# Optimization experiments

Hardware: AMD Instinct MI355X
Metric: run time of the kernel (lower is better)

## Reference

```python
import jax, jax.numpy as jnp
import numpy as np

D = 1024   # feature_dim
K = 10     # num_anchors
B = 16384  # batch
H = 8      # num_heads


def setup_inputs() -> dict:
    key = jax.random.key(0)
    ks = jax.random.split(key, 12)
    f32 = jnp.float32

    def w(k, shape, scale=0.02):
        return (jax.random.normal(k, shape, f32) * scale)

    return {
        "features": jax.random.normal(ks[0], (B, D), f32),
        "anchors": w(ks[1], (K, D), 0.1),
        # anchor_refiner: Linear(D, D//2) -> ReLU -> Linear(D//2, D) -> Tanh
        "ar_w1": w(ks[2], (D, D // 2)), "ar_b1": jnp.zeros((D // 2,), f32),
        "ar_w2": w(ks[3], (D // 2, D)), "ar_b2": jnp.zeros((D,), f32),
        # attention projections
        "q_w": w(ks[4], (D, D)), "q_b": jnp.zeros((D,), f32),
        "k_w": w(ks[5], (D, D)), "k_b": jnp.zeros((D,), f32),
        "v_w": w(ks[6], (D, D)), "v_b": jnp.zeros((D,), f32),
        "o_w": w(ks[7], (D, D)), "o_b": jnp.zeros((D,), f32),
        # feature_enhancer: LayerNorm -> Linear(D,2D) -> GELU -> Linear(2D,D)
        "ln_g": jnp.ones((D,), f32), "ln_b": jnp.zeros((D,), f32),
        "ff_w1": w(ks[8], (D, 2 * D)), "ff_b1": jnp.zeros((2 * D,), f32),
        "ff_w2": w(ks[9], (2 * D, D)), "ff_b2": jnp.zeros((D,), f32),
        "div_w": jnp.asarray(0.001, f32),
        "cen_w": jnp.asarray(0.001, f32),
    }


def _l2norm(x, eps=1e-8):
    n = jnp.linalg.norm(x, axis=-1, keepdims=True)
    return x / jnp.maximum(n, eps)


def _layernorm(x, g, b, eps=1e-5):
    mu = jnp.mean(x, axis=-1, keepdims=True)
    var = jnp.mean(jnp.square(x - mu), axis=-1, keepdims=True)
    return (x - mu) * jax.lax.rsqrt(var + eps) * g + b


def reference(features, anchors, ar_w1, ar_b1, ar_w2, ar_b2,
              q_w, q_b, k_w, k_b, v_w, v_b, o_w, o_b,
              ln_g, ln_b, ff_w1, ff_b1, ff_w2, ff_b2, div_w, cen_w):
    b = features.shape[0]
    hd = D // H
    fn = _l2norm(features)                                 # [B, D]

    # anchor refinement
    refin = jnp.tanh(jax.nn.relu(anchors @ ar_w1 + ar_b1) @ ar_w2 + ar_b2)
    an = _l2norm(anchors + 0.1 * refin)                    # [K, D]

    # multi-head cross-attention to anchors
    q = (fn @ q_w + q_b).reshape(b, H, hd)                 # [B, H, hd]
    k = (an @ k_w + k_b).reshape(K, H, hd)                 # [K, H, hd]
    v = (an @ v_w + v_b).reshape(K, H, hd)
    scores = jnp.einsum('bhd,khd->bhk', q, k) / jnp.sqrt(jnp.asarray(hd, fn.dtype))
    aw = jax.nn.softmax(scores, axis=-1)                   # [B, H, K]
    att = jnp.einsum('bhk,khd->bhd', aw, v).reshape(b, D)
    att = att @ o_w + o_b

    # feature enhancer (dropout inactive: eval mode)
    enh = fn + 0.1 * att
    h = jax.nn.gelu(_layernorm(enh, ln_g, ln_b) @ ff_w1 + ff_b1, approximate=False)
    enh = h @ ff_w2 + ff_b2
    final = fn + 0.2 * enh                                 # [B, D]

    # diversity loss: pdist over K=10 anchors (45 pairs)
    diff = an[:, None, :] - an[None, :, :]                 # [K, K, D]
    dmat = jnp.sqrt(jnp.maximum(jnp.sum(diff * diff, -1), 1e-24))
    iu = np.triu_indices(K, 1)
    div_loss = jnp.exp(-jnp.maximum(dmat[iu].mean(), 1e-6))

    # center loss: attention-weighted feature-anchor distances
    avg_att = aw.mean(axis=1)                              # [B, K]
    sq = (jnp.sum(fn * fn, 1, keepdims=True) + jnp.sum(an * an, 1)
          - 2.0 * fn @ an.T)
    fa_dist = jnp.sqrt(jnp.maximum(sq, 1e-12))             # [B, K]
    center_loss = jnp.sum(avg_att * fa_dist, axis=1).mean()

    geo = jnp.abs(div_w) * div_loss + jnp.abs(cen_w) * center_loss
    geo = jnp.clip(geo, 0.0, 0.01)
    return final, geo
```

## Files before the change

### kernel.cpp

```cpp
#include <hip/hip_runtime.h>
#include <hip/hip_bf16.h>
#include <math.h>

typedef __hip_bfloat16 bf16;

#define D_  1024
#define K_  10
#define B_  16384
#define H_  8
#define HD_ 128

struct alignas(16) BF8 { bf16 v[8]; };
struct alignas(8)  BF4 { bf16 v[4]; };

typedef __bf16 bf8v __attribute__((ext_vector_type(8)));
typedef float  f4v  __attribute__((ext_vector_type(4)));

__device__ __forceinline__ float b2f(bf16 x){ return __bfloat162float(x); }
__device__ __forceinline__ bf16  f2b(float x){ return __float2bfloat16(x); }

#define GL2LDS16(g, l) __builtin_amdgcn_global_load_lds( \
    (__attribute__((address_space(1))) void*)(g), \
    (__attribute__((address_space(3))) void*)(l), 16, 0, 0)

__global__ __launch_bounds__(256) void l2norm_k(const float* __restrict__ x,
                                                bf16* __restrict__ fnb) {
  int b = blockIdx.x, t = threadIdx.x;
  float4 v = ((const float4*)(x + (size_t)b * D_))[t];
  float p = v.x*v.x + v.y*v.y + v.z*v.z + v.w*v.w;
  #pragma unroll
  for (int o = 32; o > 0; o >>= 1) p += __shfl_down(p, o);
  __shared__ float wsum[4];
  if ((t & 63) == 0) wsum[t >> 6] = p;
  __syncthreads();
  __shared__ float inv_s;
  if (t == 0) inv_s = 1.f / fmaxf(sqrtf(wsum[0]+wsum[1]+wsum[2]+wsum[3]), 1e-8f);
  __syncthreads();
  float iv = inv_s;
  BF4 o;
  o.v[0] = f2b(v.x*iv); o.v[1] = f2b(v.y*iv);
  o.v[2] = f2b(v.z*iv); o.v[3] = f2b(v.w*iv);
  ((BF4*)(fnb + (size_t)b * D_))[t] = o;
}

__global__ __launch_bounds__(256) void wt_k(const float* __restrict__ w,
                                            bf16* __restrict__ wt, int R, int C) {
  __shared__ float tle[32][33];
  int c0 = blockIdx.x * 32, r0 = blockIdx.y * 32;
  int tx = threadIdx.x & 31, ty = threadIdx.x >> 5;
  #pragma unroll
  for (int i = 0; i < 32; i += 8)
    tle[ty + i][tx] = w[(size_t)(r0 + ty + i) * C + c0 + tx];
  __syncthreads();
  #pragma unroll
  for (int i = 0; i < 32; i += 8)
    wt[(size_t)(c0 + ty + i) * R + r0 + tx] = f2b(tle[tx][ty + i]);
}

template<int COLS, int KD, int ACT>
__global__ __launch_bounds__(256) void panelmm_k(
    const float* __restrict__ A, const float* __restrict__ W,
    const float* __restrict__ bias, const float* __restrict__ aux,
    float* __restrict__ out,
    const float* __restrict__ W2, const float* __restrict__ bias2,
    float* __restrict__ out2, int N, int npanel) {
  constexpr int GROUPS = 256 / COLS;
  constexpr int DCH = KD / GROUPS;
  __shared__ float A_s[K_][KD];
  __shared__ float part[K_][COLS][GROUPS];
  const int t = threadIdx.x;
  int blk = blockIdx.x;
  const float* Wm = W; const float* bm = bias; float* om = out;
  if (blk >= npanel) { blk -= npanel; Wm = W2; bm = bias2; om = out2; }
  const int panel = blk;
  for (int i = t; i < K_*KD; i += 256) A_s[0][i] = A[i];
  __syncthreads();
  const int cg = t % COLS, g = t / COLS;
  const int col = panel*COLS + cg;
  float s[K_];
  #pragma unroll
  for (int r = 0; r < K_; ++r) s[r] = 0.f;
  const float* wp = Wm + (size_t)(g*DCH)*N + col;
  for (int d = g*DCH; d < (g+1)*DCH; ++d) {
    float wv = *wp; wp += N;
    #pragma unroll
    for (int r = 0; r < K_; ++r) s[r] = fmaf(A_s[r][d], wv, s[r]);
  }
  #pragma unroll
  for (int r = 0; r < K_; ++r) part[r][cg][g] = s[r];
  __syncthreads();
  for (int o = t; o < K_*COLS; o += 256) {
    int r = o / COLS, c = o % COLS;
    float v = 0.f;
    #pragma unroll
    for (int gg = 0; gg < GROUPS; ++gg) v += part[r][c][gg];
    v += bm[panel*COLS + c];
    if constexpr (ACT == 1) v = fmaxf(v, 0.f);
    if constexpr (ACT == 2) v = aux[(size_t)r*N + panel*COLS + c] + 0.1f*tanhf(v);
    om[(size_t)r*N + panel*COLS + c] = v;
  }
}

template<int TRANSOUT, typename TW>
__global__ __launch_bounds__(256) void smallmm_k(
    const float* __restrict__ A, const TW* __restrict__ W,
    bf16* __restrict__ outb, float scale) {
  constexpr int COLS = 64, GROUPS = 4, DCH = 32, NW = 1024;
  __shared__ float A_s[K_][128];
  __shared__ float part[K_][COLS][GROUPS];
  const int t = threadIdx.x;
  const int h = blockIdx.x & 7, panel = blockIdx.x >> 3;
  for (int i = t; i < K_*128; i += 256) {
    int r = i >> 7, j = i & 127;
    A_s[r][j] = A[r*1024 + h*128 + j];
  }
  __syncthreads();
  const int cg = t % COLS, g = t / COLS;
  const int col = panel*COLS + cg;
  float s[K_];
  #pragma unroll
  for (int r = 0; r < K_; ++r) s[r] = 0.f;
  const TW* wp = W + (size_t)(h*128 + g*DCH)*NW + col;
  for (int d = g*DCH; d < g*DCH + DCH; ++d) {
    float wv;
    if constexpr (sizeof(TW) == 2) wv = b2f(*wp); else wv = *wp;
    wp += NW;
    #pragma unroll
    for (int r = 0; r < K_; ++r) s[r] = fmaf(A_s[r][d], wv, s[r]);
  }
  #pragma unroll
  for (int r = 0; r < K_; ++r) part[r][cg][g] = s[r];
  __syncthreads();
  for (int o = t; o < 16*COLS; o += 256) {
    int r = o / COLS, c = o % COLS;
    float v = 0.f;
    if (r < K_) {
      #pragma unroll
      for (int gg = 0; gg < GROUPS; ++gg) v += part[r][c][gg];
      v *= scale;
    }
    if constexpr (TRANSOUT) outb[(size_t)(panel*COLS + c)*128 + h*16 + r] = f2b(v);
    else                    outb[(size_t)(h*16 + r)*NW + panel*COLS + c] = f2b(v);
  }
}

__global__ void sbias_k(const float* __restrict__ qb, const float* __restrict__ Km,
                        const float* __restrict__ na, float* __restrict__ sb) {
  int c = threadIdx.x;
  if (c < 128) {
    int h = c >> 4, k = c & 15;
    float s = 0.f;
    if (k < K_) {
      for (int j = 0; j < HD_; ++j)
        s = fmaf(qb[h*HD_ + j], Km[(size_t)k*D_ + h*HD_ + j], s);
    }
    sb[c] = s * 0.08838834764831845f;
  } else {
    int j = c - 128;
    sb[c] = (j < K_) ? (1.f + na[j]) : 0.f;
  }
}

__global__ __launch_bounds__(256) void anext_k(const float* __restrict__ an,
                                               bf16* __restrict__ wt) {
  int k = blockIdx.x;
  bf16* dst = wt + (size_t)(128 + k) * 1024;
  int i = threadIdx.x * 4;
  BF4 o;
  if (k < K_) {
    float4 a = *(const float4*)(an + (size_t)k*1024 + i);
    o.v[0] = f2b(-2.f*a.x); o.v[1] = f2b(-2.f*a.y);
    o.v[2] = f2b(-2.f*a.z); o.v[3] = f2b(-2.f*a.w);
  } else {
    o.v[0] = o.v[1] = o.v[2] = o.v[3] = f2b(0.f);
  }
  *(BF4*)(dst + i) = o;
}

__global__ __launch_bounds__(256) void ar3_k(const float* __restrict__ an_un,
    float* __restrict__ an, float* __restrict__ na, float* __restrict__ divloss) {
  __shared__ float a_s[K_][D_];
  __shared__ float nrm[K_];
  __shared__ float dm[45];
  const int t = threadIdx.x;
  for (int i = t; i < K_*D_; i += 256) a_s[0][i] = an_un[i];
  __syncthreads();
  const int wid = t >> 6, lane = t & 63;
  for (int r = wid; r < K_; r += 4) {
    float p = 0.f;
    for (int j = lane; j < D_; j += 64) p += a_s[r][j]*a_s[r][j];
    #pragma unroll
    for (int o = 1; o < 64; o <<= 1) p += __shfl_xor(p, o);
    if (lane == 0) nrm[r] = p;
  }
  __syncthreads();
  for (int i = t; i < K_*D_; i += 256) {
    int r = i >> 10;
    float iv = 1.f / fmaxf(sqrtf(nrm[r]), 1e-8f);
    float v = a_s[0][i] * iv;
    a_s[0][i] = v;
    an[i] = v;
  }
  if (t < K_) {
    float iv = 1.f / fmaxf(sqrtf(nrm[t]), 1e-8f);
    na[t] = nrm[t] * iv * iv;
  }
  __syncthreads();
  const int pr = t >> 2, sub = t & 3;
  if (pr < 45) {
    int i = 0, j = 0, c = pr;
    for (i = 0; i < K_; ++i) { int cnt = K_-1-i; if (c < cnt) { j = i+1+c; break; } c -= cnt; }
    float s = 0.f;
    for (int d = sub*256; d < sub*256 + 256; ++d) {
      float df = a_s[i][d] - a_s[j][d]; s += df*df;
    }
    s += __shfl_xor(s, 1); s += __shfl_xor(s, 2);
    if (sub == 0) dm[pr] = sqrtf(fmaxf(s, 1e-24f));
  }
  __syncthreads();
  if (t == 0) {
    float m = 0.f;
    for (int p = 0; p < 45; ++p) m += dm[p];
    m *= (1.f/45.f);
    *divloss = expf(-fmaxf(m, 1e-6f));
  }
}

template<int EPI, typename TO>
__global__ __launch_bounds__(256) void mgemm_k(
    const bf16* __restrict__ A, const bf16* __restrict__ Bt,
    const float* __restrict__ bias, const bf16* __restrict__ aux,
    TO* __restrict__ out, int M, int N, int Kd, float scale) {
  constexpr int BM = 128, BN = 128, BK = 32;
  __shared__ bf16 As[BM][BK];
  __shared__ bf16 Bs[BN][BK];
  const int tid = threadIdx.x;
  const int nMB = M / BM;
  const int nwg = gridDim.x;
  int wg = blockIdx.x;
  wg = (wg & 7) * (nwg >> 3) + (wg >> 3);
  const int mb = wg % nMB, nb = wg / nMB;
  const int bm = mb * BM, bn = nb * BN;

  const int srow = tid >> 2;
  const int sk   = (tid & 3) * 8;
  const bf16* ga = A  + (size_t)(bm + srow) * Kd + sk;
  const bf16* gb = Bt + (size_t)(bn + srow) * Kd + sk;
  const size_t rstep = (size_t)64 * Kd;
  bf16* la = &As[0][0] + tid * 8;
  bf16* lb = &Bs[0][0] + tid * 8;

  const int w    = tid >> 6;
  const int lane = tid & 63;
  const int wr = (w >> 1) * 64, wc = (w & 1) * 64;
  const int fr = lane & 15, fg = lane >> 4;

  f4v acc[4][4];
  const f4v zz = {0.f, 0.f, 0.f, 0.f};
  #pragma unroll
  for (int m = 0; m < 4; ++m)
    #pragma unroll
    for (int n = 0; n < 4; ++n) acc[m][n] = zz;

  for (int k0 = 0; k0 < Kd; k0 += BK) {
    GL2LDS16(ga,         la);
    GL2LDS16(ga + rstep, la + 2048);
    GL2LDS16(gb,         lb);
    GL2LDS16(gb + rstep, lb + 2048);
    __syncthreads();
    bf8v af[4], bf_[4];
    #pragma unroll
    for (int m = 0; m < 4; ++m)
      af[m] = *(const bf8v*)&As[wr + m*16 + fr][fg*8];
    #pragma unroll
    for (int n = 0; n < 4; ++n)
      bf_[n] = *(const bf8v*)&Bs[wc + n*16 + fr][fg*8];
    #pragma unroll
    for (int m = 0; m < 4; ++m)
      #pragma unroll
      for (int n = 0; n < 4; ++n)
        acc[m][n] = __builtin_amdgcn_mfma_f32_16x16x32_bf16(af[m], bf_[n], acc[m][n], 0, 0, 0);
    __syncthreads();
    ga += BK; gb += BK;
  }

  float bv[4];
  #pragma unroll
  for (int n = 0; n < 4; ++n) bv[n] = bias[bn + wc + n*16 + fr];
  #pragma unroll
  for (int m = 0; m < 4; ++m) {
    #pragma unroll
    for (int r = 0; r < 4; ++r) {
      const int row = bm + wr + m*16 + fg*4 + r;
      #pragma unroll
      for (int n = 0; n < 4; ++n) {
        const int col = bn + wc + n*16 + fr;
        float x = acc[m][n][r] + bv[n];
        if constexpr (EPI == 1) x = b2f(aux[(size_t)row * N + col]) + scale * x;
        if constexpr (EPI == 2) x = 0.5f * x * (1.f + erff(x * 0.70710678118654752f));
        if constexpr (sizeof(TO) == 2) out[(size_t)row * N + col] = f2b(x);
        else                           out[(size_t)row * N + col] = x;
      }
    }
  }
}

template<int EPI, typename TO>
__global__ __launch_bounds__(512) void mgemm256_k(
    const bf16* __restrict__ A, const bf16* __restrict__ Bt,
    const float* __restrict__ bias, const bf16* __restrict__ aux,
    TO* __restrict__ out, int M, int N, int Kd, float scale) {
  constexpr int BM = 256, BN = 256, BK = 64;
  __shared__ bf16 As[2][BM*BK];
  __shared__ bf16 Bs[2][BN*BK];
  const int tid = threadIdx.x;
  const int nMB = M / BM;
  const int nwg = gridDim.x;
  int wg = blockIdx.x;
  wg = (wg & 7) * (nwg >> 3) + (wg >> 3);
  const int bm = (wg % nMB) * BM, bn = (wg / nMB) * BN;

  const int srow = tid >> 3;
  const int scsw = ((tid & 7) ^ (srow & 7)) * 8;
  const bf16* gA = A  + (size_t)(bm + srow) * Kd + scsw;
  const bf16* gB = Bt + (size_t)(bn + srow) * Kd + scsw;
  const size_t lstep = (size_t)64 * Kd;

  const int wid = tid >> 6, lane = tid & 63;
  const int wm = wid >> 2, wn = wid & 3;
  const int fr = lane & 15, fg = lane >> 4;
  const int fsw = fr & 7;

  f4v acc[8][4];
  const f4v zz = {0.f, 0.f, 0.f, 0.f};
  #pragma unroll
  for (int m = 0; m < 8; ++m)
    #pragma unroll
    for (int n = 0; n < 4; ++n) acc[m][n] = zz;

  const int nt = Kd / BK;

  #pragma unroll
  for (int l = 0; l < 4; ++l) {
    GL2LDS16(gA + l*lstep, &As[0][0] + tid*8 + l*4096);
    GL2LDS16(gB + l*lstep, &Bs[0][0] + tid*8 + l*4096);
  }
  __syncthreads();

  int buf = 0;
  for (int t = 0; t < nt; ++t) {
    if (t + 1 < nt) {
      const int ko = (t + 1) * BK;
      #pragma unroll
      for (int l = 0; l < 4; ++l) {
        GL2LDS16(gA + l*lstep + ko, &As[buf^1][0] + tid*8 + l*4096);
        GL2LDS16(gB + l*lstep + ko, &Bs[buf^1][0] + tid*8 + l*4096);
      }
    }
    const bf16* la = &As[buf][0];
    const bf16* lb = &Bs[buf][0];
    bf8v bq[8];
    #pragma unroll
    for (int n = 0; n < 4; ++n) {
      const int rb = wn*64 + n*16 + fr;
      bq[n*2]   = *(const bf8v*)(lb + rb*64 + ((fg     ^ fsw) * 8));
      bq[n*2+1] = *(const bf8v*)(lb + rb*64 + (((4+fg) ^ fsw) * 8));
    }
    __builtin_amdgcn_s_setprio(1);
    #pragma unroll
    for (int m = 0; m < 8; ++m) {
      const int ra = wm*128 + m*16 + fr;
      bf8v a0 = *(const bf8v*)(la + ra*64 + ((fg     ^ fsw) * 8));
      bf8v a1 = *(const bf8v*)(la + ra*64 + (((4+fg) ^ fsw) * 8));
      #pragma unroll
      for (int n = 0; n < 4; ++n) {
        acc[m][n] = __builtin_amdgcn_mfma_f32_16x16x32_bf16(a0, bq[n*2],   acc[m][n], 0, 0, 0);
        acc[m][n] = __builtin_amdgcn_mfma_f32_16x16x32_bf16(a1, bq[n*2+1], acc[m][n], 0, 0, 0);
      }
    }
    __builtin_amdgcn_s_setprio(0);
    __syncthreads();
    buf ^= 1;
  }

  float bv[4];
  #pragma unroll
  for (int n = 0; n < 4; ++n) bv[n] = bias[bn + wn*64 + n*16 + fr];
  #pragma unroll
  for (int m = 0; m < 8; ++m) {
    #pragma unroll
    for (int r = 0; r < 4; ++r) {
      const int row = bm + wm*128 + m*16 + fg*4 + r;
      #pragma unroll
      for (int n = 0; n < 4; ++n) {
        const int col = bn + wn*64 + n*16 + fr;
        float x = acc[m][n][r] + bv[n];
        if constexpr (EPI == 1) x = b2f(aux[(size_t)row * N + col]) + scale * x;
        if constexpr (EPI == 2) x = 0.5f * x * (1.f + erff(x * 0.70710678118654752f));
        if constexpr (sizeof(TO) == 2) out[(size_t)row * N + col] = f2b(x);
        else                           out[(size_t)row * N + col] = x;
      }
    }
  }
}

__global__ __launch_bounds__(256) void attn2_k(
    const float* __restrict__ S, bf16* __restrict__ awp,
    float* __restrict__ cen_acc) {
  __shared__ float cred[4];
  const int t = threadIdx.x;
  const int wid = t >> 6, lane = t & 63;
  const int sub = lane & 7, head = lane >> 3;
  const int k0 = sub*2, k1 = k0 + 1;
  float c_acc = 0.f;
  const int row0 = blockIdx.x * 32 + wid * 8;

  for (int i = 0; i < 8; ++i) {
    const int row = row0 + i;
    const float* Sr = S + (size_t)row * 256;
    float2 sv = *(const float2*)(Sr + head*16 + k0);
    float v0 = (k0 < K_) ? sv.x : -1e30f;
    float v1 = (k1 < K_) ? sv.y : -1e30f;
    float m = fmaxf(v0, v1);
    m = fmaxf(m, __shfl_xor(m,1)); m = fmaxf(m, __shfl_xor(m,2)); m = fmaxf(m, __shfl_xor(m,4));
    float e0 = (k0 < K_) ? __expf(v0 - m) : 0.f;
    float e1 = (k1 < K_) ? __expf(v1 - m) : 0.f;
    float es = e0 + e1;
    es += __shfl_xor(es,1); es += __shfl_xor(es,2); es += __shfl_xor(es,4);
    float inv = 1.f / es;
    float a0 = e0 * inv, a1 = e1 * inv;
    bf16 b0 = f2b(a0), b1 = f2b(a1);
    unsigned int pk = (unsigned int)(*(unsigned short*)&b0)
                    | ((unsigned int)(*(unsigned short*)&b1) << 16);
    *(unsigned int*)(awp + (size_t)row*128 + head*16 + k0) = pk;
    float g0 = a0, g1 = a1;
    g0 += __shfl_xor(g0,8); g0 += __shfl_xor(g0,16); g0 += __shfl_xor(g0,32);
    g1 += __shfl_xor(g1,8); g1 += __shfl_xor(g1,16); g1 += __shfl_xor(g1,32);
    if (sub < 5) {
      float d20 = Sr[128 + k0];
      float d21 = Sr[128 + k1];
      c_acc = fmaf(g0, sqrtf(fmaxf(d20, 1e-12f)), c_acc);
      c_acc = fmaf(g1, sqrtf(fmaxf(d21, 1e-12f)), c_acc);
    }
  }
  #pragma unroll
  for (int o = 1; o < 64; o <<= 1) c_acc += __shfl_xor(c_acc, o);
  if (lane == 0) cred[wid] = c_acc;
  __syncthreads();
  if (t == 0) {
    float s = (cred[0]+cred[1]+cred[2]+cred[3]) * (1.f/64.f/(float)B_);
    atomicAdd(cen_acc, s);
  }
}

__global__ __launch_bounds__(256) void ln_k(const bf16* __restrict__ x,
    const float* __restrict__ g, const float* __restrict__ bta,
    bf16* __restrict__ out) {
  int b = blockIdx.x, t = threadIdx.x;
  BF4 ld = ((const BF4*)(x + (size_t)b * D_))[t];
  float v[4];
  #pragma unroll
  for (int j = 0; j < 4; ++j) v[j] = b2f(ld.v[j]);
  float s = v[0]+v[1]+v[2]+v[3];
  #pragma unroll
  for (int o = 32; o > 0; o >>= 1) s += __shfl_down(s, o);
  __shared__ float w1[4], w2[4];
  if ((t & 63) == 0) w1[t >> 6] = s;
  __syncthreads();
  __shared__ float mu_s, rs_s;
  if (t == 0) mu_s = (w1[0]+w1[1]+w1[2]+w1[3]) * (1.f/D_);
  __syncthreads();
  float mu = mu_s;
  float qv = 0.f;
  #pragma unroll
  for (int j = 0; j < 4; ++j) { float d = v[j]-mu; qv += d*d; }
  #pragma unroll
  for (int o = 32; o > 0; o >>= 1) qv += __shfl_down(qv, o);
  if ((t & 63) == 0) w2[t >> 6] = qv;
  __syncthreads();
  if (t == 0) rs_s = rsqrtf((w2[0]+w2[1]+w2[2]+w2[3]) * (1.f/D_) + 1e-5f);
  __syncthreads();
  float rs = rs_s;
  BF4 o;
  #pragma unroll
  for (int j = 0; j < 4; ++j) {
    int col = t*4 + j;
    o.v[j] = f2b((v[j]-mu)*rs*g[col] + bta[col]);
  }
  ((BF4*)(out + (size_t)b * D_))[t] = o;
}

__global__ void geo_k(const float* __restrict__ divl, const float* __restrict__ cen,
                      const float* __restrict__ div_w, const float* __restrict__ cen_w,
                      float* __restrict__ out) {
  float g = fabsf(*div_w) * (*divl) + fabsf(*cen_w) * (*cen);
  out[0] = fminf(fmaxf(g, 0.f), 0.01f);
}

extern "C" void kernel_launch(void* const* d_in, const int* in_sizes, int n_in,
                              void* d_out, int out_size, void* d_ws, size_t ws_size,
                              hipStream_t stream) {
  const float* features = (const float*)d_in[0];
  const float* anchors  = (const float*)d_in[1];
  const float* ar_w1 = (const float*)d_in[2];
  const float* ar_b1 = (const float*)d_in[3];
  const float* ar_w2 = (const float*)d_in[4];
  const float* ar_b2 = (const float*)d_in[5];
  const float* q_w = (const float*)d_in[6];
  const float* q_b = (const float*)d_in[7];
  const float* k_w = (const float*)d_in[8];
  const float* k_b = (const float*)d_in[9];
  const float* v_w = (const float*)d_in[10];
  const float* v_b = (const float*)d_in[11];
  const float* o_w = (const float*)d_in[12];
  const float* o_b = (const float*)d_in[13];
  const float* ln_g = (const float*)d_in[14];
  const float* ln_b = (const float*)d_in[15];
  const float* ff_w1 = (const float*)d_in[16];
  const float* ff_b1 = (const float*)d_in[17];
  const float* ff_w2 = (const float*)d_in[18];
  const float* ff_b2 = (const float*)d_in[19];
  const float* div_w = (const float*)d_in[20];
  const float* cen_w = (const float*)d_in[21];
  float* out = (float*)d_out;

  char* w = (char*)d_ws;
  bf16* ws_fnb = (bf16*)w;  w += (size_t)B_ * D_ * 2;
  bf16* ws_enh = (bf16*)w;  w += (size_t)B_ * D_ * 2;
  bf16* ws_ln  = (bf16*)w;  w += (size_t)B_ * D_ * 2;
  bf16* ws_h   = (bf16*)w;  w += (size_t)B_ * 2048 * 2;
  float* ws_S  = (float*)w; w += (size_t)B_ * 256 * 4;
  bf16* ws_awp = (bf16*)w;  w += (size_t)B_ * 128 * 2;
  bf16* ws_wq  = (bf16*)w;  w += (size_t)D_ * D_ * 2;
  bf16* ws_w1t = (bf16*)w;  w += (size_t)D_ * 2048 * 2;
  bf16* ws_w2t = (bf16*)w;  w += (size_t)2048 * D_ * 2;
  bf16* ws_wt  = (bf16*)w;  w += (size_t)256 * D_ * 2;
  bf16* ws_vt  = (bf16*)w;  w += (size_t)D_ * 128 * 2;
  float* ws_har = (float*)w;  w += (size_t)K_ * (D_/2) * 4;
  float* ws_anu = (float*)w;  w += (size_t)K_ * D_ * 4;
  float* ws_an  = (float*)w;  w += (size_t)K_ * D_ * 4;
  float* ws_k   = (float*)w;  w += (size_t)K_ * D_ * 4;
  float* ws_v   = (float*)w;  w += (size_t)K_ * D_ * 4;
  float* ws_na  = (float*)w;  w += 256;
  float* ws_div = (float*)w;  w += 256;
  float* ws_cen = (float*)w;  w += 256;
  float* ws_sb  = (float*)w;  w += 512;
  if ((size_t)(w - (char*)d_ws) > ws_size) return;

  hipMemsetAsync(ws_cen, 0, 4, stream);

  wt_k<<<dim3(D_/32,   D_/32),   256, 0, stream>>>(q_w,   ws_wq,  D_,   D_);
  wt_k<<<dim3(2048/32, D_/32),   256, 0, stream>>>(ff_w1, ws_w1t, D_,   2048);
  wt_k<<<dim3(D_/32,   2048/32), 256, 0, stream>>>(ff_w2, ws_w2t, 2048, D_);

  l2norm_k<<<B_, 256, 0, stream>>>(features, ws_fnb);

  panelmm_k<32, 1024, 1><<<16, 256, 0, stream>>>(
      anchors, ar_w1, ar_b1, nullptr, ws_har,
      nullptr, nullptr, nullptr, D_/2, 16);
  panelmm_k<64, 512, 2><<<16, 256, 0, stream>>>(
      ws_har, ar_w2, ar_b2, anchors, ws_anu,
      nullptr, nullptr, nullptr, D_, 16);
  ar3_k<<<1, 256, 0, stream>>>(ws_anu, ws_an, ws_na, ws_div);
  panelmm_k<64, 1024, 0><<<32, 256, 0, stream>>>(
      ws_an, k_w, k_b, nullptr, ws_k,
      v_w, v_b, ws_v, D_, 16);

  smallmm_k<0, bf16><<<128, 256, 0, stream>>>(ws_k, ws_wq, ws_wt, 0.08838834764831845f);
  anext_k<<<128, 256, 0, stream>>>(ws_an, ws_wt);
  sbias_k<<<1, 256, 0, stream>>>(q_b, ws_k, ws_na, ws_sb);
  smallmm_k<1, float><<<128, 256, 0, stream>>>(ws_v, o_w, ws_vt, 1.f);

  mgemm_k<0, float><<<dim3((B_/128)*(256/128)), 256, 0, stream>>>(
      ws_fnb, ws_wt, ws_sb, nullptr, ws_S, B_, 256, D_, 0.f);

  attn2_k<<<B_/32, 256, 0, stream>>>(ws_S, ws_awp, ws_cen);

  mgemm256_k<1, bf16><<<dim3((B_/256)*(D_/256)), 512, 0, stream>>>(
      ws_awp, ws_vt, o_b, ws_fnb, ws_enh, B_, D_, 128, 0.1f);

  ln_k<<<B_, 256, 0, stream>>>(ws_enh, ln_g, ln_b, ws_ln);

  mgemm256_k<2, bf16><<<dim3((B_/256)*(2048/256)), 512, 0, stream>>>(
      ws_ln, ws_w1t, ff_b1, nullptr, ws_h, B_, 2048, D_, 0.f);

  mgemm256_k<1, float><<<dim3((B_/256)*(D_/256)), 512, 0, stream>>>(
      ws_h, ws_w2t, ff_b2, ws_fnb, out, B_, D_, 2048, 0.2f);

  geo_k<<<1, 1, 0, stream>>>(ws_div, ws_cen, div_w, cen_w, out + (size_t)B_ * D_);
}
```

Before: 420.0 us.

## Replace 256x256 GEMM with double-buffered swizzled 128x128 tile kernel

Removes the 256x256x64 MFMA GEMM and rewrites the 128x128x32 kernel with LDS double buffering and an XOR swizzle to reduce bank conflicts. The three large GEMMs (out-proj, FF1, FF2) now launch the smaller-tile kernel with 256 threads. This aims for higher occupancy and more workgroups, at the cost of halving per-tile data reuse and adding more global and LDS traffic per FLOP.

```diff
diff --git a/kernel.cpp b/kernel.cpp
--- a/kernel.cpp
+++ b/kernel.cpp
@@ -232,85 +232,6 @@
     const float* __restrict__ bias, const bf16* __restrict__ aux,
     TO* __restrict__ out, int M, int N, int Kd, float scale) {
   constexpr int BM = 128, BN = 128, BK = 32;
-  __shared__ bf16 As[BM][BK];
-  __shared__ bf16 Bs[BN][BK];
-  const int tid = threadIdx.x;
-  const int nMB = M / BM;
-  const int nwg = gridDim.x;
-  int wg = blockIdx.x;
-  wg = (wg & 7) * (nwg >> 3) + (wg >> 3);
-  const int mb = wg % nMB, nb = wg / nMB;
-  const int bm = mb * BM, bn = nb * BN;
-
-  const int srow = tid >> 2;
-  const int sk   = (tid & 3) * 8;
-  const bf16* ga = A  + (size_t)(bm + srow) * Kd + sk;
-  const bf16* gb = Bt + (size_t)(bn + srow) * Kd + sk;
-  const size_t rstep = (size_t)64 * Kd;
-  bf16* la = &As[0][0] + tid * 8;
-  bf16* lb = &Bs[0][0] + tid * 8;
-
-  const int w    = tid >> 6;
-  const int lane = tid & 63;
-  const int wr = (w >> 1) * 64, wc = (w & 1) * 64;
-  const int fr = lane & 15, fg = lane >> 4;
-
-  f4v acc[4][4];
-  const f4v zz = {0.f, 0.f, 0.f, 0.f};
-  #pragma unroll
-  for (int m = 0; m < 4; ++m)
-    #pragma unroll
-    for (int n = 0; n < 4; ++n) acc[m][n] = zz;
-
-  for (int k0 = 0; k0 < Kd; k0 += BK) {
-    GL2LDS16(ga,         la);
-    GL2LDS16(ga + rstep, la + 2048);
-    GL2LDS16(gb,         lb);
-    GL2LDS16(gb + rstep, lb + 2048);
-    __syncthreads();
-    bf8v af[4], bf_[4];
-    #pragma unroll
-    for (int m = 0; m < 4; ++m)
-      af[m] = *(const bf8v*)&As[wr + m*16 + fr][fg*8];
-    #pragma unroll
-    for (int n = 0; n < 4; ++n)
-      bf_[n] = *(const bf8v*)&Bs[wc + n*16 + fr][fg*8];
-    #pragma unroll
-    for (int m = 0; m < 4; ++m)
-      #pragma unroll
-      for (int n = 0; n < 4; ++n)
-        acc[m][n] = __builtin_amdgcn_mfma_f32_16x16x32_bf16(af[m], bf_[n], acc[m][n], 0, 0, 0);
-    __syncthreads();
-    ga += BK; gb += BK;
-  }
-
-  float bv[4];
-  #pragma unroll
-  for (int n = 0; n < 4; ++n) bv[n] = bias[bn + wc + n*16 + fr];
-  #pragma unroll
-  for (int m = 0; m < 4; ++m) {
-    #pragma unroll
-    for (int r = 0; r < 4; ++r) {
-      const int row = bm + wr + m*16 + fg*4 + r;
-      #pragma unroll
-      for (int n = 0; n < 4; ++n) {
-        const int col = bn + wc + n*16 + fr;
-        float x = acc[m][n][r] + bv[n];
-        if constexpr (EPI == 1) x = b2f(aux[(size_t)row * N + col]) + scale * x;
-        if constexpr (EPI == 2) x = 0.5f * x * (1.f + erff(x * 0.70710678118654752f));
-        if constexpr (sizeof(TO) == 2) out[(size_t)row * N + col] = f2b(x);
-        else                           out[(size_t)row * N + col] = x;
-      }
-    }
-  }
-}
-
-template<int EPI, typename TO>
-__global__ __launch_bounds__(512) void mgemm256_k(
-    const bf16* __restrict__ A, const bf16* __restrict__ Bt,
-    const float* __restrict__ bias, const bf16* __restrict__ aux,
-    TO* __restrict__ out, int M, int N, int Kd, float scale) {
-  constexpr int BM = 256, BN = 256, BK = 64;
   __shared__ bf16 As[2][BM*BK];
   __shared__ bf16 Bs[2][BN*BK];
   const int tid = threadIdx.x;
@@ -320,64 +241,57 @@
   wg = (wg & 7) * (nwg >> 3) + (wg >> 3);
   const int bm = (wg % nMB) * BM, bn = (wg / nMB) * BN;
 
-  const int srow = tid >> 3;
-  const int scsw = ((tid & 7) ^ (srow & 7)) * 8;
-  const bf16* gA = A  + (size_t)(bm + srow) * Kd + scsw;
-  const bf16* gB = Bt + (size_t)(bn + srow) * Kd + scsw;
-  const size_t lstep = (size_t)64 * Kd;
-
-  const int wid = tid >> 6, lane = tid & 63;
-  const int wm = wid >> 2, wn = wid & 3;
+  const int srow = tid >> 2;
+  const int ssw  = (((tid & 3) ^ ((tid >> 3) & 3)) * 8);
+  const bf16* gA = A  + (size_t)(bm + srow) * Kd + ssw;
+  const bf16* gB = Bt + (size_t)(bn + srow) * Kd + ssw;
+  const size_t rstep = (size_t)64 * Kd;
+
+  const int w    = tid >> 6;
+  const int lane = tid & 63;
+  const int wr = (w >> 1) * 64, wc = (w & 1) * 64;
   const int fr = lane & 15, fg = lane >> 4;
-  const int fsw = fr & 7;
-
-  f4v acc[8][4];
+  const int key = (fr >> 1) & 3;
+
+  f4v acc[4][4];
   const f4v zz = {0.f, 0.f, 0.f, 0.f};
   #pragma unroll
-  for (int m = 0; m < 8; ++m)
+  for (int m = 0; m < 4; ++m)
     #pragma unroll
     for (int n = 0; n < 4; ++n) acc[m][n] = zz;
 
   const int nt = Kd / BK;
 
-  #pragma unroll
-  for (int l = 0; l < 4; ++l) {
-    GL2LDS16(gA + l*lstep, &As[0][0] + tid*8 + l*4096);
-    GL2LDS16(gB + l*lstep, &Bs[0][0] + tid*8 + l*4096);
-  }
+  GL2LDS16(gA,         &As[0][0] + tid*8);
+  GL2LDS16(gA + rstep, &As[0][0] + tid*8 + 2048);
+  GL2LDS16(gB,         &Bs[0][0] + tid*8);
+  GL2LDS16(gB + rstep, &Bs[0][0] + tid*8 + 2048);
   __syncthreads();
 
   int buf = 0;
   for (int t = 0; t < nt; ++t) {
     if (t + 1 < nt) {
       const int ko = (t + 1) * BK;
-      #pragma unroll
-      for (int l = 0; l < 4; ++l) {
-        GL2LDS16(gA + l*lstep + ko, &As[buf^1][0] + tid*8 + l*4096);
-        GL2LDS16(gB + l*lstep + ko, &Bs[buf^1][0] + tid*8 + l*4096);
-      }
+      GL2LDS16(gA + ko,         &As[buf^1][0] + tid*8);
+      GL2LDS16(gA + rstep + ko, &As[buf^1][0] + tid*8 + 2048);
+      GL2LDS16(gB + ko,         &Bs[buf^1][0] + tid*8);
+      GL2LDS16(gB + rstep + ko, &Bs[buf^1][0] + tid*8 + 2048);
     }
     const bf16* la = &As[buf][0];
     const bf16* lb = &Bs[buf][0];
-    bf8v bq[8];
-    #pragma unroll
-    for (int n = 0; n < 4; ++n) {
-      const int rb = wn*64 + n*16 + fr;
-      bq[n*2]   = *(const bf8v*)(lb + rb*64 + ((fg     ^ fsw) * 8));
-      bq[n*2+1] = *(const bf8v*)(lb + rb*64 + (((4+fg) ^ fsw) * 8));
-    }
+    bf8v af[4], bq[4];
+    #pragma unroll
+    for (int m = 0; m < 4; ++m)
+      af[m] = *(const bf8v*)(la + (wr + m*16 + fr)*BK + ((fg ^ key) * 8));
+    #pragma unroll
+    for (int n = 0; n < 4; ++n)
+      bq[n] = *(const bf8v*)(lb + (wc + n*16 + fr)*BK + ((fg ^ key) * 8));
     __builtin_amdgcn_s_setprio(1);
     #pragma unroll
-    for (int m = 0; m < 8; ++m) {
-      const int ra = wm*128 + m*16 + fr;
-      bf8v a0 = *(const bf8v*)(la + ra*64 + ((fg     ^ fsw) * 8));
-      bf8v a1 = *(const bf8v*)(la + ra*64 + (((4+fg) ^ fsw) * 8));
+    for (int m = 0; m < 4; ++m)
       #pragma unroll
-      for (int n = 0; n < 4; ++n) {
-        acc[m][n] = __builtin_amdgcn_mfma_f32_16x16x32_bf16(a0, bq[n*2],   acc[m][n], 0, 0, 0);
-        acc[m][n] = __builtin_amdgcn_mfma_f32_16x16x32_bf16(a1, bq[n*2+1], acc[m][n], 0, 0, 0);
-      }
-    }
+      for (int n = 0; n < 4; ++n)
+        acc[m][n] = __builtin_amdgcn_mfma_f32_16x16x32_bf16(af[m], bq[n], acc[m][n], 0, 0, 0);
     __builtin_amdgcn_s_setprio(0);
     __syncthreads();
     buf ^= 1;
@@ -385,15 +299,15 @@
 
   float bv[4];
   #pragma unroll
-  for (int n = 0; n < 4; ++n) bv[n] = bias[bn + wn*64 + n*16 + fr];
-  #pragma unroll
-  for (int m = 0; m < 8; ++m) {
+  for (int n = 0; n < 4; ++n) bv[n] = bias[bn + wc + n*16 + fr];
+  #pragma unroll
+  for (int m = 0; m < 4; ++m) {
     #pragma unroll
     for (int r = 0; r < 4; ++r) {
-      const int row = bm + wm*128 + m*16 + fg*4 + r;
+      const int row = bm + wr + m*16 + fg*4 + r;
       #pragma unroll
       for (int n = 0; n < 4; ++n) {
-        const int col = bn + wn*64 + n*16 + fr;
+        const int col = bn + wc + n*16 + fr;
         float x = acc[m][n][r] + bv[n];
         if constexpr (EPI == 1) x = b2f(aux[(size_t)row * N + col]) + scale * x;
         if constexpr (EPI == 2) x = 0.5f * x * (1.f + erff(x * 0.70710678118654752f));
@@ -576,15 +490,15 @@
 
   attn2_k<<<B_/32, 256, 0, stream>>>(ws_S, ws_awp, ws_cen);
 
-  mgemm256_k<1, bf16><<<dim3((B_/256)*(D_/256)), 512, 0, stream>>>(
+  mgemm_k<1, bf16><<<dim3((B_/128)*(D_/128)), 256, 0, stream>>>(
       ws_awp, ws_vt, o_b, ws_fnb, ws_enh, B_, D_, 128, 0.1f);
 
   ln_k<<<B_, 256, 0, stream>>>(ws_enh, ln_g, ln_b, ws_ln);
 
-  mgemm256_k<2, bf16><<<dim3((B_/256)*(2048/256)), 512, 0, stream>>>(
+  mgemm_k<2, bf16><<<dim3((B_/128)*(2048/128)), 256, 0, stream>>>(
       ws_ln, ws_w1t, ff_b1, nullptr, ws_h, B_, 2048, D_, 0.f);
 
-  mgemm256_k<1, float><<<dim3((B_/256)*(D_/256)), 512, 0, stream>>>(
+  mgemm_k<1, float><<<dim3((B_/128)*(D_/128)), 256, 0, stream>>>(
       ws_h, ws_w2t, ff_b2, ws_fnb, out, B_, D_, 2048, 0.2f);
 
   geo_k<<<1, 1, 0, stream>>>(ws_div, ws_cen, div_w, cen_w, out + (size_t)B_ * D_);
```

Measured after the change: 452.3 us. +7.7%, slower.
